# Optimization experiments

Measured on AMD Instinct MI355X. Metric: run time of the kernel, lower is better.

The kernel has to match this reference:

```python
import jax, jax.numpy as jnp
import numpy as np

H = 1024     # hidden_size
NH = 16      # num heads
HD = H // NH # head_dim = 64
I = 4096     # intermediate_size
EPS = 1e-6


def rmsnorm(x, w, eps=EPS):
    var = jnp.mean(jnp.square(x), axis=-1, keepdims=True)
    return x * jax.lax.rsqrt(var + eps) * w


def attention(x, ctx, wq, wk, wv, wo):
    # x: [B,S,H], ctx: [B,Skv,H]; weights stored [in,out]
    B, S, _ = x.shape
    Skv = ctx.shape[1]
    q = (x @ wq).reshape(B, S, NH, HD)
    k = (ctx @ wk).reshape(B, Skv, NH, HD)
    v = (ctx @ wv).reshape(B, Skv, NH, HD)
    scores = jnp.einsum('bqhd,bkhd->bhqk', q, k) * (HD ** -0.5)
    attn = jax.nn.softmax(scores.astype(jnp.float32), axis=-1).astype(q.dtype)
    out = jnp.einsum('bhqk,bkhd->bqhd', attn, v).reshape(B, S, NH * HD)
    return out @ wo


def mlp(x, wg, wu, wd):
    return (jax.nn.silu(x @ wg) * (x @ wu)) @ wd


def setup_inputs() -> dict:
    key = jax.random.key(0)
    ks = jax.random.split(key, 16)
    p = lambda k, shape: (jax.random.normal(k, shape, jnp.float32) * 0.02)
    return {
        'hidden_states': jax.random.normal(ks[0], (1, 2048, H), jnp.float32),
        'context': jax.random.normal(ks[1], (1, 2048, H), jnp.float32),
        'sa_norm_w': jnp.ones((H,), jnp.float32),
        'sa_wq': p(ks[2], (H, NH * HD)),
        'sa_wk': p(ks[3], (H, NH * HD)),
        'sa_wv': p(ks[4], (H, NH * HD)),
        'sa_wo': p(ks[5], (NH * HD, H)),
        'ca_norm_w': jnp.ones((H,), jnp.float32),
        'ca_wq': p(ks[6], (H, NH * HD)),
        'ca_wk': p(ks[7], (H, NH * HD)),
        'ca_wv': p(ks[8], (H, NH * HD)),
        'ca_wo': p(ks[9], (NH * HD, H)),
        'mlp_norm_w': jnp.ones((H,), jnp.float32),
        'w_gate': p(ks[10], (H, I)),
        'w_up': p(ks[11], (H, I)),
        'w_down': p(ks[12], (I, H)),
    }


def reference(hidden_states, context, sa_norm_w, sa_wq, sa_wk, sa_wv, sa_wo,
              ca_norm_w, ca_wq, ca_wk, ca_wv, ca_wo,
              mlp_norm_w, w_gate, w_up, w_down):
    # self-attention block
    residual = hidden_states
    h = rmsnorm(hidden_states, sa_norm_w)
    h = residual + attention(h, h, sa_wq, sa_wk, sa_wv, sa_wo)
    # cross-attention block
    residual = h
    hn = rmsnorm(h, ca_norm_w)
    h = residual + attention(hn, context, ca_wq, ca_wk, ca_wv, ca_wo)
    # MLP block
    residual = h
    hn = rmsnorm(h, mlp_norm_w)
    h = residual + mlp(hn, w_gate, w_up, w_down)
    return h
```

## Files before the change

### kernel.cpp

```cpp
#include <hip/hip_runtime.h>

#define H 1024
#define S 2048
#define NH 16
#define HD 64
#define ISZ 4096

typedef __attribute__((ext_vector_type(8))) short s8v;
typedef __attribute__((ext_vector_type(4))) short s4v;
typedef __attribute__((ext_vector_type(4))) float f4v;
typedef __attribute__((ext_vector_type(2))) unsigned u2v;

#define MFMA16 __builtin_amdgcn_mfma_f32_16x16x32_bf16

__device__ __forceinline__ short f2bf(float f) {
    unsigned u = __builtin_bit_cast(unsigned, f);
    unsigned r = (u + 0x7FFFu + ((u >> 16) & 1u)) >> 16;
    return (short)r;
}
__device__ __forceinline__ float bf2f(short s) {
    unsigned u = ((unsigned)(unsigned short)s) << 16;
    return __builtin_bit_cast(float, u);
}
__device__ __forceinline__ float exp2_hw(float x) {
    float r; asm("v_exp_f32 %0, %1" : "=v"(r) : "v"(x)); return r;
}
__device__ __forceinline__ unsigned cvt_pk_bf16(float lo, float hi) {
    unsigned r; asm("v_cvt_pk_bf16_f32 %0, %1, %2" : "=v"(r) : "v"(lo), "v"(hi)); return r;
}

__device__ __forceinline__ void gload_lds16(const short* g, short* l) {
    __builtin_amdgcn_global_load_lds(
        (const __attribute__((address_space(1))) void*)g,
        (__attribute__((address_space(3))) void*)l, 16, 0, 0);
}

template <int N> struct VMt { static constexpr int val = N; };

struct PreArgs {
    const void* hid; const void* ctx;
    const void* sanw; const void* canw; const void* mlpnw;
    const void* w[11];
    short* hidc; short* ctxc; short* xn;
    short* canw_o; short* mlpnw_o;
    short* wT[11];
    int* flag_out;
};

__device__ __forceinline__ void tr_tile(const void* src, short* dst, int K, int N,
                                        int k0, int n0, int rmul, int roff,
                                        int isbf, float* tile ) {
    int t = threadIdx.x;
    int c = t & 31, r0 = t >> 5;
    if (isbf) {
        const short* s = (const short*)src;
#pragma unroll
        for (int i = 0; i < 4; i++)
            tile[(r0 + i * 8) * 33 + c] = bf2f(s[(k0 + r0 + i * 8) * N + n0 + c]);
    } else {
        const float* s = (const float*)src;
#pragma unroll
        for (int i = 0; i < 4; i++)
            tile[(r0 + i * 8) * 33 + c] = s[(k0 + r0 + i * 8) * N + n0 + c];
    }
    __syncthreads();
#pragma unroll
    for (int i = 0; i < 4; i++)
        dst[((n0 + r0 + i * 8) * rmul + roff) * K + k0 + c] = f2bf(tile[c * 33 + r0 + i * 8]);
}

__global__ __launch_bounds__(256) void preamble_kernel(PreArgs pa) {
    __shared__ float tile[32 * 33];
    __shared__ float red[4];
    int b = blockIdx.x;
    int t = threadIdx.x;
    int isbf = (((const unsigned*)pa.sanw)[0] == 0x3F803F80u);
    if (blockIdx.x == 0 && t == 0) pa.flag_out[0] = isbf;

    if (b < 2048) {
        int row = b;
        float xf[4];
        if (isbf) {
            s4v xv = *(const s4v*)((const short*)pa.hid + row * H + t * 4);
#pragma unroll
            for (int j = 0; j < 4; j++) xf[j] = bf2f(xv[j]);
        } else {
            const float* s = (const float*)pa.hid + row * H + t * 4;
#pragma unroll
            for (int j = 0; j < 4; j++) xf[j] = s[j];
        }
        float ss = 0.f;
        s4v cv;
#pragma unroll
        for (int j = 0; j < 4; j++) { cv[j] = f2bf(xf[j]); xf[j] = bf2f(cv[j]); ss += xf[j] * xf[j]; }
        *(s4v*)(pa.hidc + row * H + t * 4) = cv;
        int lane = t & 63, wid = t >> 6;
#pragma unroll
        for (int off = 32; off >= 1; off >>= 1) ss += __shfl_xor(ss, off);
        if (lane == 0) red[wid] = ss;
        __syncthreads();
        float tot = red[0] + red[1] + red[2] + red[3];
        float scale = rsqrtf(tot * (1.f / (float)H) + 1e-6f);
        float wv[4];
        if (isbf) {
            s4v wq = *(const s4v*)((const short*)pa.sanw + t * 4);
#pragma unroll
            for (int j = 0; j < 4; j++) wv[j] = bf2f(wq[j]);
        } else {
            const float* s = (const float*)pa.sanw + t * 4;
#pragma unroll
            for (int j = 0; j < 4; j++) wv[j] = s[j];
        }
        s4v ov;
#pragma unroll
        for (int j = 0; j < 4; j++) ov[j] = f2bf(xf[j] * scale * wv[j]);
        *(s4v*)(pa.xn + row * H + t * 4) = ov;
        return;
    }
    b -= 2048;
    if (b < 1024) {
        int i8 = b * 2048 + t * 8;
        if (isbf) {
            *(s8v*)(pa.ctxc + i8) = *(const s8v*)((const short*)pa.ctx + i8);
        } else {
            const float* s = (const float*)pa.ctx;
            s8v o;
#pragma unroll
            for (int j = 0; j < 8; j++) o[j] = f2bf(s[i8 + j]);
            *(s8v*)(pa.ctxc + i8) = o;
        }
        return;
    }
    b -= 1024;
    if (b < 2) {
        const void* src = (b == 0) ? pa.canw : pa.mlpnw;
        short* dst = (b == 0) ? pa.canw_o : pa.mlpnw_o;
        if (isbf) { if (t * 4 < H) *(s4v*)(dst + t * 4) = *(const s4v*)((const short*)src + t * 4); }
        else {
            const float* s = (const float*)src;
            s4v o;
#pragma unroll
            for (int j = 0; j < 4; j++) o[j] = f2bf(s[t * 4 + j]);
            *(s4v*)(dst + t * 4) = o;
        }
        return;
    }
    b -= 2;
    if (b < 8 * 1024) {
        int w = b >> 10, tl = b & 1023;
        tr_tile(pa.w[w], pa.wT[w], H, H, (tl & 31) * 32, (tl >> 5) * 32, 1, 0, isbf, tile);
        return;
    }
    b -= 8 * 1024;
    if (b < 2 * 4096) {
        int w = 8 + (b >> 12), tl = b & 4095;
        tr_tile(pa.w[w], pa.wT[8], H, ISZ, (tl & 31) * 32, (tl >> 5) * 32, 2, w - 8, isbf, tile);
        return;
    }
    b -= 2 * 4096;
    {
        tr_tile(pa.w[10], pa.wT[10], ISZ, H, (b & 127) * 32, (b >> 7) * 32, 1, 0, isbf, tile);
    }
}

__global__ __launch_bounds__(256) void rmsnorm_kernel(const short* __restrict__ x,
                                                      const short* __restrict__ w,
                                                      short* __restrict__ out) {
    int row = blockIdx.x;
    int t = threadIdx.x;
    int lane = t & 63, wid = t >> 6;
    const short* xr = x + row * H;

    s4v xv = *(const s4v*)(xr + t * 4);
    float xf[4];
    float ss = 0.f;
#pragma unroll
    for (int j = 0; j < 4; j++) { xf[j] = bf2f(xv[j]); ss += xf[j] * xf[j]; }
#pragma unroll
    for (int off = 32; off >= 1; off >>= 1) ss += __shfl_xor(ss, off);

    __shared__ float red[4];
    if (lane == 0) red[wid] = ss;
    __syncthreads();
    float tot = red[0] + red[1] + red[2] + red[3];
    float scale = rsqrtf(tot * (1.f / (float)H) + 1e-6f);

    s4v wv = *(const s4v*)(w + t * 4);
    s4v ov;
#pragma unroll
    for (int j = 0; j < 4; j++) ov[j] = f2bf(xf[j] * scale * bf2f(wv[j]));
    *(s4v*)(out + row * H + t * 4) = ov;
}

template <int BM_, int BN_>
__global__ __launch_bounds__(512, 2) void gemm_bt_kernel(
    const short* __restrict__ A0, const short* __restrict__ A1, int split, int lda,
    const short* __restrict__ Bt,
    void* __restrict__ C, int ldc, int K,
    const short* __restrict__ res,
    const int* __restrict__ dtype_flag,
    short* __restrict__ vtbuf, int vcol0,
    short* __restrict__ silu_out) {

    constexpr int MC = BM_ / 32;
    constexpr int NC = BN_ / 64;
    constexpr int U  = (BM_ + BN_) / 8;
    constexpr int PT = U / 8;
    constexpr int BUF = (BM_ + BN_) * 64;

    __shared__ short lds[2 * BUF];

    const short* A = (blockIdx.y < split) ? A0 : A1;
    int m0 = blockIdx.x * BM_;
    int n0 = blockIdx.y * BN_;

    int t = threadIdx.x;
    int lane = t & 63, wid = t >> 6;
    int quad = lane >> 4, l15 = lane & 15;
    int wr = wid >> 2, wc = wid & 3;
    int ld4 = lane >> 2, lc8 = (lane & 3) * 8;

    f4v acc[MC][NC] = {};

    auto stage = [&](short* buf, int k0) {
#pragma unroll
        for (int s = 0; s < PT; ++s) {
            int u = wid * PT + s;
            if (u < BM_ / 8) {
                int h = u / (BM_ / 16), r16 = u % (BM_ / 16);
                gload_lds16(A + (m0 + r16 * 16 + ld4) * lda + k0 + h * 32 + lc8,
                            buf + h * (BM_ * 32) + r16 * 512);
            } else {
                int ub = u - BM_ / 8;
                int h = ub / (BN_ / 16), r16 = ub % (BN_ / 16);
                gload_lds16(Bt + (n0 + r16 * 16 + ld4) * K + k0 + h * 32 + lc8,
                            buf + BM_ * 64 + h * (BN_ * 32) + r16 * 512);
            }
        }
    };

    auto compute = [&](const short* buf) {
#pragma unroll
        for (int kh = 0; kh < 2; ++kh) {
            s8v af[MC], bfv[NC];
#pragma unroll
            for (int mc = 0; mc < MC; ++mc)
                af[mc] = *(const s8v*)(buf + kh * (BM_ * 32) +
                                       (wr * (BM_ / 2) + mc * 16 + l15) * 32 + quad * 8);
#pragma unroll
            for (int nc = 0; nc < NC; ++nc)
                bfv[nc] = *(const s8v*)(buf + BM_ * 64 + kh * (BN_ * 32) +
                                        (wc * (BN_ / 4) + nc * 16 + l15) * 32 + quad * 8);
#pragma unroll
            for (int mc = 0; mc < MC; ++mc)
#pragma unroll
                for (int nc = 0; nc < NC; ++nc)
                    acc[mc][nc] = MFMA16(af[mc], bfv[nc], acc[mc][nc], 0, 0, 0);
        }
    };

    const int KT = K / 64;
    stage(lds, 0);
    __syncthreads();
    int cur = 0;
    for (int kt = 0; kt < KT - 1; ++kt) {
        stage(lds + (cur ^ 1) * BUF, (kt + 1) * 64);
        compute(lds + cur * BUF);
        __syncthreads();
        cur ^= 1;
    }
    compute(lds + cur * BUF);

    if (silu_out) {
#pragma unroll
        for (int mc = 0; mc < MC; mc++) {
#pragma unroll
            for (int nc = 0; nc < NC; nc++) {
                int row = m0 + wr * (BM_ / 2) + mc * 16 + quad * 4;
                int col = n0 + wc * (BN_ / 4) + nc * 16 + l15;
#pragma unroll
                for (int r = 0; r < 4; r++) {
                    float v = acc[mc][nc][r];
                    float other = __shfl_xor(v, 1);
                    if ((l15 & 1) == 0) {
                        float sig = 1.f / (1.f + __expf(-v));
                        silu_out[(row + r) * ISZ + (col >> 1)] = f2bf(v * sig * other);
                    }
                }
            }
        }
        return;
    }

    int out_fp32 = (dtype_flag != nullptr) && (dtype_flag[0] == 0);

#pragma unroll
    for (int mc = 0; mc < MC; mc++) {
#pragma unroll
        for (int nc = 0; nc < NC; nc++) {
            int row = m0 + wr * (BM_ / 2) + mc * 16 + quad * 4;
            int col = n0 + wc * (BN_ / 4) + nc * 16 + l15;
#pragma unroll
            for (int r = 0; r < 4; r++) {
                float vf = acc[mc][nc][r];
                if (res) vf += bf2f(res[(row + r) * ldc + col]);
                if (vtbuf && col >= vcol0)
                    vtbuf[(col - vcol0) * S + row + r] = f2bf(vf);
                else if (out_fp32)
                    ((float*)C)[(row + r) * ldc + col] = vf;
                else
                    ((short*)C)[(row + r) * ldc + col] = f2bf(vf);
            }
        }
    }
}

template <int BM_, int BN_>
__global__ __launch_bounds__(512, 2) void gemm_np_kernel(
    const short* __restrict__ A, int lda,
    const short* __restrict__ Bt,
    void* __restrict__ C, int ldc, int K,
    const short* __restrict__ res,
    const int* __restrict__ dtype_flag) {

    constexpr int MC = BM_ / 32;
    constexpr int NC = BN_ / 64;
    constexpr int PT = (BM_ + BN_) / 64;
    constexpr int BUF = (BM_ + BN_) * 64;

    __shared__ short lds[4 * BUF];

    int lin = blockIdx.x;
    int sw = (lin & 7) * 32 + (lin >> 3);
    int m0 = (sw & 31) * BM_;
    int n0 = (sw >> 5) * BN_;

    int t_ = threadIdx.x;
    int lane = t_ & 63, wid = t_ >> 6;
    int quad = lane >> 4, l15 = lane & 15;
    int wr = wid >> 2, wc = wid & 3;
    int ld4 = lane >> 2;
    int lcs = (((lane & 3) ^ ((ld4 >> 1) & 3)) * 8);
    int sq  = quad ^ ((l15 >> 1) & 3);

    f4v acc[MC][NC] = {};

    auto stage = [&](int bi, int kt) {
        short* buf = lds + bi * BUF;
        int k0 = kt * 64;
#pragma unroll
        for (int s = 0; s < PT; ++s) {
            int u = wid * PT + s;
            if (u < BM_ / 8) {
                int hh = u / (BM_ / 16), r16 = u % (BM_ / 16);
                gload_lds16(A + (m0 + r16 * 16 + ld4) * lda + k0 + hh * 32 + lcs,
                            buf + hh * (BM_ * 32) + r16 * 512);
            } else {
                int ub = u - BM_ / 8;
                int hh = ub / (BN_ / 16), r16 = ub % (BN_ / 16);
                gload_lds16(Bt + (n0 + r16 * 16 + ld4) * K + k0 + hh * 32 + lcs,
                            buf + BM_ * 64 + hh * (BN_ * 32) + r16 * 512);
            }
        }
    };

    auto tile = [&](int t, auto wt) {
        constexpr int W = decltype(wt)::val;
        if constexpr (W == 9)      asm volatile("s_waitcnt vmcnt(9)" ::: "memory");
        else if constexpr (W == 6) asm volatile("s_waitcnt vmcnt(6)" ::: "memory");
        else if constexpr (W == 3) asm volatile("s_waitcnt vmcnt(3)" ::: "memory");
        else                       asm volatile("s_waitcnt vmcnt(0)" ::: "memory");
        __builtin_amdgcn_s_barrier();
        const short* bc = lds + (t & 3) * BUF;
        s8v af[2][MC], bv[2][NC];
#pragma unroll
        for (int kh = 0; kh < 2; ++kh) {
#pragma unroll
            for (int mc = 0; mc < MC; ++mc)
                af[kh][mc] = *(const s8v*)(bc + kh * (BM_ * 32) +
                                           (wr * (BM_ / 2) + mc * 16 + l15) * 32 + sq * 8);
#pragma unroll
            for (int nc = 0; nc < NC; ++nc)
                bv[kh][nc] = *(const s8v*)(bc + BM_ * 64 + kh * (BN_ * 32) +
                                           (wc * (BN_ / 4) + nc * 16 + l15) * 32 + sq * 8);
        }
        asm volatile("s_waitcnt lgkmcnt(0)" ::: "memory");
        __builtin_amdgcn_s_barrier();
        __builtin_amdgcn_s_setprio(1);
#pragma unroll
        for (int kh = 0; kh < 2; ++kh)
#pragma unroll
            for (int mc = 0; mc < MC; ++mc)
#pragma unroll
                for (int nc = 0; nc < NC; ++nc)
                    acc[mc][nc] = MFMA16(af[kh][mc], bv[kh][nc], acc[mc][nc], 0, 0, 0);
        __builtin_amdgcn_s_setprio(0);
    };

    const int KT = K / 64;
    stage(0, 0); stage(1, 1); stage(2, 2);
    for (int t = 0; t < KT - 3; ++t) {
        stage((t + 3) & 3, t + 3);
        tile(t, VMt<9>{});
    }
    tile(KT - 3, VMt<6>{});
    tile(KT - 2, VMt<3>{});
    tile(KT - 1, VMt<0>{});

    int out_fp32 = (dtype_flag != nullptr) && (dtype_flag[0] == 0);
#pragma unroll
    for (int mc = 0; mc < MC; mc++) {
#pragma unroll
        for (int nc = 0; nc < NC; nc++) {
            int row = m0 + wr * (BM_ / 2) + mc * 16 + quad * 4;
            int col = n0 + wc * (BN_ / 4) + nc * 16 + l15;
#pragma unroll
            for (int r = 0; r < 4; r++) {
                float vf = acc[mc][nc][r];
                if (res) vf += bf2f(res[(row + r) * ldc + col]);
                if (out_fp32)
                    ((float*)C)[(row + r) * ldc + col] = vf;
                else
                    ((short*)C)[(row + r) * ldc + col] = f2bf(vf);
            }
        }
    }
}

__global__ __launch_bounds__(512, 2) void gemm_gu8_kernel(
    const short* __restrict__ A, const short* __restrict__ Bt,
    short* __restrict__ silu_out) {

    __shared__ short lds[65536];

    int lin = blockIdx.x;
    int sw = (lin & 7) * 32 + (lin >> 3);
    int m0 = (sw & 7) * 256;
    int n0 = (sw >> 3) * 256;

    int t = threadIdx.x;
    int lane = t & 63, wid = t >> 6;
    int quad = lane >> 4, l15 = lane & 15;
    int wr = wid >> 2, wc = wid & 3;
    int ld4 = lane >> 2;
    int lcs = (((lane & 3) ^ ((ld4 >> 1) & 3)) * 8);
    int sq  = quad ^ ((l15 >> 1) & 3);

    f4v acc[8][4] = {};

    const short* Arow = A + (m0 + ld4) * 1024 + lcs;
    const short* Brow = Bt + (n0 + ld4) * 1024 + lcs;

    auto stA = [&](int buf, int kt, int kh) {
        short* d = lds + buf * 32768 + kh * 8192;
#pragma unroll
        for (int i = 0; i < 2; i++) {
            int r0 = (wid + 8 * i) * 16;
            gload_lds16(Arow + r0 * 1024 + kt * 64 + kh * 32, d + r0 * 32);
        }
    };
    auto stB = [&](int buf, int kt, int kh) {
        short* d = lds + buf * 32768 + 16384 + kh * 8192;
#pragma unroll
        for (int i = 0; i < 2; i++) {
            int r0 = (wid + 8 * i) * 16;
            gload_lds16(Brow + r0 * 1024 + kt * 64 + kh * 32, d + r0 * 32);
        }
    };

    const int aoff = (wr * 128 + l15) * 32 + sq * 8;
    const int boff = 16384 + (wc * 64 + l15) * 32 + sq * 8;

    stA(0, 0, 0); stB(0, 0, 0); stA(0, 0, 1); stB(0, 0, 1);
    asm volatile("s_waitcnt vmcnt(4)" ::: "memory");
    __builtin_amdgcn_s_barrier();

    int cur = 0;
    for (int kt = 0; kt < 15; ++kt) {
        const short* bc = lds + cur * 32768;
        int nb = cur ^ 1;
        s8v af[8], b0, b1;

#pragma unroll
        for (int mc = 0; mc < 8; ++mc) af[mc] = *(const s8v*)(bc + aoff + mc * 512);
        b0 = *(const s8v*)(bc + boff);
        b1 = *(const s8v*)(bc + boff + 512);
        stA(nb, kt + 1, 0);
        __builtin_amdgcn_s_barrier();
        asm volatile("s_waitcnt lgkmcnt(0)" ::: "memory");
        __builtin_amdgcn_s_setprio(1);
#pragma unroll
        for (int mc = 0; mc < 8; ++mc) {
            acc[mc][0] = MFMA16(af[mc], b0, acc[mc][0], 0, 0, 0);
            acc[mc][1] = MFMA16(af[mc], b1, acc[mc][1], 0, 0, 0);
        }
        __builtin_amdgcn_s_setprio(0);
        __builtin_amdgcn_s_barrier();

        b0 = *(const s8v*)(bc + boff + 1024);
        b1 = *(const s8v*)(bc + boff + 1536);
        stB(nb, kt + 1, 0);
        asm volatile("s_waitcnt vmcnt(4)" ::: "memory");
        __builtin_amdgcn_s_barrier();
        asm volatile("s_waitcnt lgkmcnt(0)" ::: "memory");
        __builtin_amdgcn_s_setprio(1);
#pragma unroll
        for (int mc = 0; mc < 8; ++mc) {
            acc[mc][2] = MFMA16(af[mc], b0, acc[mc][2], 0, 0, 0);
            acc[mc][3] = MFMA16(af[mc], b1, acc[mc][3], 0, 0, 0);
        }
        __builtin_amdgcn_s_setprio(0);
        __builtin_amdgcn_s_barrier();

#pragma unroll
        for (int mc = 0; mc < 8; ++mc) af[mc] = *(const s8v*)(bc + 8192 + aoff + mc * 512);
        b0 = *(const s8v*)(bc + 8192 + boff);
        b1 = *(const s8v*)(bc + 8192 + boff + 512);
        stA(nb, kt + 1, 1);
        __builtin_amdgcn_s_barrier();
        asm volatile("s_waitcnt lgkmcnt(0)" ::: "memory");
        __builtin_amdgcn_s_setprio(1);
#pragma unroll
        for (int mc = 0; mc < 8; ++mc) {
            acc[mc][0] = MFMA16(af[mc], b0, acc[mc][0], 0, 0, 0);
            acc[mc][1] = MFMA16(af[mc], b1, acc[mc][1], 0, 0, 0);
        }
        __builtin_amdgcn_s_setprio(0);
        __builtin_amdgcn_s_barrier();

        b0 = *(const s8v*)(bc + 8192 + boff + 1024);
        b1 = *(const s8v*)(bc + 8192 + boff + 1536);
        stB(nb, kt + 1, 1);
        asm volatile("s_waitcnt vmcnt(4)" ::: "memory");
        __builtin_amdgcn_s_barrier();
        asm volatile("s_waitcnt lgkmcnt(0)" ::: "memory");
        __builtin_amdgcn_s_setprio(1);
#pragma unroll
        for (int mc = 0; mc < 8; ++mc) {
            acc[mc][2] = MFMA16(af[mc], b0, acc[mc][2], 0, 0, 0);
            acc[mc][3] = MFMA16(af[mc], b1, acc[mc][3], 0, 0, 0);
        }
        __builtin_amdgcn_s_setprio(0);
        __builtin_amdgcn_s_barrier();

        cur ^= 1;
    }

    asm volatile("s_waitcnt vmcnt(0)" ::: "memory");
    __builtin_amdgcn_s_barrier();
    {
        const short* bc = lds + cur * 32768;
#pragma unroll
        for (int kh = 0; kh < 2; ++kh) {
            s8v af[8], bv[4];
#pragma unroll
            for (int mc = 0; mc < 8; ++mc) af[mc] = *(const s8v*)(bc + kh * 8192 + aoff + mc * 512);
#pragma unroll
            for (int nc = 0; nc < 4; ++nc) bv[nc] = *(const s8v*)(bc + kh * 8192 + boff + nc * 512);
#pragma unroll
            for (int mc = 0; mc < 8; ++mc)
#pragma unroll
                for (int nc = 0; nc < 4; ++nc)
                    acc[mc][nc] = MFMA16(af[mc], bv[nc], acc[mc][nc], 0, 0, 0);
        }
    }

#pragma unroll
    for (int mc = 0; mc < 8; mc++) {
#pragma unroll
        for (int nc = 0; nc < 4; nc++) {
            int row = m0 + wr * 128 + mc * 16 + quad * 4;
            int col = n0 + wc * 64 + nc * 16 + l15;
#pragma unroll
            for (int r = 0; r < 4; r++) {
                float v = acc[mc][nc][r];
                float other = __shfl_xor(v, 1);
                if ((l15 & 1) == 0) {
                    float sig = 1.f / (1.f + __expf(-v));
                    silu_out[(row + r) * ISZ + (col >> 1)] = f2bf(v * sig * other);
                }
            }
        }
    }
}

__global__ __launch_bounds__(512, 4) void flash_attn_kernel(const short* __restrict__ q,
                                                            const short* __restrict__ kk,
                                                            const short* __restrict__ vt,
                                                            int rs,
                                                            short* __restrict__ o) {
    __shared__ short lds[40960];

    int h = blockIdx.y;
    int q0 = blockIdx.x * 64;
    int t = threadIdx.x;
    int lane = t & 63, wid = t >> 6;
    int quad = lane >> 4, l15 = lane & 15;
    int gw = wid & 3, gh = wid >> 2;
    int kvbase = gh * 1024;
    int kro = l15 & 7;

    int lrow = lane >> 3;
    int lsrc = ((lane & 7) ^ lrow) * 8;

    auto stageKV = [&](int buf, int tt) {
        int kvt = kvbase + tt * 64;
        short* kb = lds + (gh * 2 + buf) * 4096;
        short* vb = lds + 16384 + (gh * 2 + buf) * 4096;
#pragma unroll
        for (int i = 0; i < 2; i++) {
            int r0 = gw * 16 + i * 8;
            gload_lds16(kk + (kvt + r0 + lrow) * rs + h * HD + lsrc, kb + r0 * 64);
            gload_lds16(vt + (h * HD + r0 + lrow) * S + kvt + lsrc, vb + r0 * 64);
        }
    };

    const float qscale = 0.125f * 1.44269504f;
    s8v bq[2];
    int qrow = q0 + gw * 16 + l15;
#pragma unroll
    for (int c = 0; c < 2; c++) {
        s8v raw = *(const s8v*)(q + qrow * rs + h * HD + c * 32 + quad * 8);
#pragma unroll
        for (int j = 0; j < 8; j++) bq[c][j] = f2bf(qscale * bf2f(raw[j]));
    }

    f4v o_acc[4] = {};
    float m_s = -INFINITY, l_s = 0.f;
    short* pw = lds + 32768 + wid * 1024;

    const int NT = 16;
    stageKV(0, 0);
    __syncthreads();
    int cur = 0;
    for (int tt = 0; tt < NT; ++tt) {
        if (tt + 1 < NT) stageKV(cur ^ 1, tt + 1);
        const short* kb = lds + (gh * 2 + cur) * 4096;
        const short* vb = lds + 16384 + (gh * 2 + cur) * 4096;

        f4v st[4];
#pragma unroll
        for (int kc = 0; kc < 4; kc++) {
            f4v a_ = (f4v){0.f, 0.f, 0.f, 0.f};
#pragma unroll
            for (int dc = 0; dc < 2; dc++) {
                s8v kf = *(const s8v*)(kb + (kc * 16 + l15) * 64 + ((dc * 4 + quad) ^ kro) * 8);
                a_ = MFMA16(kf, bq[dc], a_, 0, 0, 0);
            }
            st[kc] = a_;
        }

        float mloc = -INFINITY;
#pragma unroll
        for (int kc = 0; kc < 4; kc++)
#pragma unroll
            for (int r = 0; r < 4; r++) mloc = fmaxf(mloc, st[kc][r]);
        mloc = fmaxf(mloc, __shfl_xor(mloc, 16));
        mloc = fmaxf(mloc, __shfl_xor(mloc, 32));
        float m_new = fmaxf(m_s, mloc);
        float alpha = exp2_hw(m_s - m_new);
        float lloc = 0.f;
#pragma unroll
        for (int kc = 0; kc < 4; kc++)
#pragma unroll
            for (int r = 0; r < 4; r++) {
                float p = exp2_hw(st[kc][r] - m_new);
                st[kc][r] = p;
                lloc += p;
            }
        lloc += __shfl_xor(lloc, 16);
        lloc += __shfl_xor(lloc, 32);
        l_s = l_s * alpha + lloc;
        m_s = m_new;
#pragma unroll
        for (int nd = 0; nd < 4; nd++)
#pragma unroll
            for (int r = 0; r < 4; r++) o_acc[nd][r] *= alpha;

#pragma unroll
        for (int kc = 0; kc < 4; kc++) {
            u2v w;
            w[0] = cvt_pk_bf16(st[kc][0], st[kc][1]);
            w[1] = cvt_pk_bf16(st[kc][2], st[kc][3]);
            int pslot = (kc * 2 + (quad >> 1)) ^ kro;
            *(u2v*)(pw + l15 * 64 + pslot * 8 + (quad & 1) * 4) = w;
        }

#pragma unroll
        for (int nd = 0; nd < 4; nd++) {
#pragma unroll
            for (int kc2 = 0; kc2 < 2; kc2++) {
                s8v vf = *(const s8v*)(vb + (nd * 16 + l15) * 64 + ((kc2 * 4 + quad) ^ kro) * 8);
                s8v pf = *(const s8v*)(pw + l15 * 64 + ((kc2 * 4 + quad) ^ kro) * 8);
                o_acc[nd] = MFMA16(vf, pf, o_acc[nd], 0, 0, 0);
            }
        }
        __syncthreads();
        cur ^= 1;
    }

    float* ex = (float*)lds;
    if (gh == 1) {
        int base = (gw * 64 + lane) * 20;
#pragma unroll
        for (int nd = 0; nd < 4; nd++) *(f4v*)(ex + base + nd * 4) = o_acc[nd];
        ex[base + 16] = m_s;
        ex[base + 17] = l_s;
    }
    __syncthreads();
    if (gh == 1) return;

    int base = (wid * 64 + lane) * 20;
    float mB = ex[base + 16], lB = ex[base + 17];
    float M = fmaxf(m_s, mB);
    float a = exp2_hw(m_s - M), bsc = exp2_hw(mB - M);
    float inv = 1.f / (a * l_s + bsc * lB);
#pragma unroll
    for (int nd = 0; nd < 4; nd++) {
        f4v ob = *(const f4v*)(ex + base + nd * 4);
#pragma unroll
        for (int r = 0; r < 4; r++)
            o_acc[nd][r] = (a * o_acc[nd][r] + bsc * ob[r]) * inv;
    }

#pragma unroll
    for (int nd = 0; nd < 4; nd++)
#pragma unroll
        for (int r = 0; r < 4; r++)
            pw[l15 * 64 + nd * 16 + quad * 4 + r] = f2bf(o_acc[nd][r]);

    int qr = lane >> 2, dc2 = (lane & 3) * 16;
    s8v x0 = *(const s8v*)(pw + qr * 64 + dc2);
    s8v x1 = *(const s8v*)(pw + qr * 64 + dc2 + 8);
    short* dst = o + (q0 + wid * 16 + qr) * H + h * HD + dc2;
    *(s8v*)(dst) = x0;
    *(s8v*)(dst + 8) = x1;
}

extern "C" void kernel_launch(void* const* d_in, const int* in_sizes, int n_in,
                              void* d_out, int out_size, void* d_ws, size_t ws_size,
                              hipStream_t stream) {
    const int SH = S * H;
    const int WH = H * H;
    const int WI = H * ISZ;

    int* flag = (int*)d_ws;
    short* base = (short*)d_ws + 16;

    short* hidc   = base;
    short* ctxc   = hidc + SH;
    short* sanw   = ctxc + SH;
    short* canw   = sanw + H;
    short* mlpnw  = canw + H;
    short* saqkvT = mlpnw + H;
    short* sawoT  = saqkvT + 3 * WH;
    short* caqkvT = sawoT + WH;
    short* cawoT  = caqkvT + 3 * WH;
    short* wguT   = cawoT + WH;
    short* wdT    = wguT + 2 * WI;
    short* xn     = wdT + WI;
    short* qkv    = xn + SH;
    short* ao     = qkv + 3 * SH;
    short* h1     = ao + SH;
    short* gu     = qkv;
    short* h2     = qkv + 8 * SH;
    short* vt     = h2 + SH;

    dim3 blk(256);
    dim3 blk2(512);

    PreArgs pa;
    pa.hid = d_in[0]; pa.ctx = d_in[1];
    pa.sanw = d_in[2]; pa.canw = d_in[7]; pa.mlpnw = d_in[12];
    const void* wsrc[11] = {d_in[3], d_in[4], d_in[5], d_in[6],
                            d_in[8], d_in[9], d_in[10], d_in[11],
                            d_in[13], d_in[14], d_in[15]};
    short* wdst[11] = {saqkvT, saqkvT + WH, saqkvT + 2 * WH, sawoT,
                       caqkvT, caqkvT + WH, caqkvT + 2 * WH, cawoT,
                       wguT, wguT , wdT};
    for (int i = 0; i < 11; i++) { pa.w[i] = wsrc[i]; pa.wT[i] = wdst[i]; }
    pa.hidc = hidc; pa.ctxc = ctxc; pa.xn = xn;
    pa.canw_o = canw; pa.mlpnw_o = mlpnw;
    pa.flag_out = flag;
    const int pre_blocks = 2048 + 1024 + 2 + 8 * 1024 + 2 * 4096 + 4096;
    preamble_kernel<<<pre_blocks, blk, 0, stream>>>(pa);

    gemm_bt_kernel<128, 128><<<dim3(S / 128, 3 * H / 128), blk2, 0, stream>>>(
        xn, xn, 24, H, saqkvT, qkv, 3 * H, H, nullptr, nullptr, vt, 2 * H, nullptr);
    flash_attn_kernel<<<dim3(S / 64, NH), blk2, 0, stream>>>(qkv, qkv + H, vt, 3 * H, ao);
    gemm_np_kernel<64, 128><<<dim3(256), blk2, 0, stream>>>(
        ao, H, sawoT, h1, H, H, hidc, nullptr);

    rmsnorm_kernel<<<S, blk, 0, stream>>>(h1, canw, xn);
    gemm_bt_kernel<128, 128><<<dim3(S / 128, 3 * H / 128), blk2, 0, stream>>>(
        xn, ctxc, 8, H, caqkvT, qkv, 3 * H, H, nullptr, nullptr, vt, 2 * H, nullptr);
    flash_attn_kernel<<<dim3(S / 64, NH), blk2, 0, stream>>>(qkv, qkv + H, vt, 3 * H, ao);
    gemm_np_kernel<64, 128><<<dim3(256), blk2, 0, stream>>>(
        ao, H, cawoT, h2, H, H, h1, nullptr);

    rmsnorm_kernel<<<S, blk, 0, stream>>>(h2, mlpnw, xn);
    gemm_gu8_kernel<<<dim3(256), blk2, 0, stream>>>(xn, wguT, gu);
    gemm_np_kernel<64, 128><<<dim3(256), blk2, 0, stream>>>(
        gu, ISZ, wdT, d_out, H, ISZ, h2, flag);
}
```

Baseline: 424.5 us.

## Vectorize weight transpose tiles and pipeline QKV GEMM and attention with fine-grained waits

The weight-transpose preamble now moves 64x32 tiles with 16-byte vector loads and stores, which halves the block count and cuts per-element memory ops. The QKV GEMM is restructured to issue all LDS fragment loads before the MFMAs, uses explicit vmcnt/lgkmcnt waits with raw barriers instead of __syncthreads, raises wave priority during the MFMA section, and drops the unused silu epilogue. Flash attention swaps its full syncs for partial vmcnt waits so the next KV prefetch stays in flight. In gemm_gu8 the LDS XOR swizzle is removed, which may add LDS bank conflicts, and the hand-counted vmcnt values must match the number of outstanding loads.

Result: no change. 425.8 us (+0.3%).

```diff
diff --git a/kernel.cpp b/kernel.cpp
--- a/kernel.cpp
+++ b/kernel.cpp
@@ -51,26 +51,32 @@
                                         int k0, int n0, int rmul, int roff,
                                         int isbf, float* tile ) {
     int t = threadIdx.x;
-    int c = t & 31, r0 = t >> 5;
     if (isbf) {
         const short* s = (const short*)src;
-#pragma unroll
-        for (int i = 0; i < 4; i++)
-            tile[(r0 + i * 8) * 33 + c] = bf2f(s[(k0 + r0 + i * 8) * N + n0 + c]);
+        int r = t >> 2, c8 = (t & 3) * 8;
+        s8v v = *(const s8v*)(s + (k0 + r) * N + n0 + c8);
+#pragma unroll
+        for (int j = 0; j < 8; j++) tile[r * 33 + c8 + j] = bf2f(v[j]);
     } else {
         const float* s = (const float*)src;
-#pragma unroll
-        for (int i = 0; i < 4; i++)
-            tile[(r0 + i * 8) * 33 + c] = s[(k0 + r0 + i * 8) * N + n0 + c];
+        int r = t >> 2, c16 = (t & 3) * 8;
+#pragma unroll
+        for (int j = 0; j < 2; j++) {
+            f4v v = *(const f4v*)(s + (k0 + r) * N + n0 + c16 + j * 4);
+#pragma unroll
+            for (int e = 0; e < 4; e++) tile[r * 33 + c16 + j * 4 + e] = v[e];
+        }
     }
     __syncthreads();
-#pragma unroll
-    for (int i = 0; i < 4; i++)
-        dst[((n0 + r0 + i * 8) * rmul + roff) * K + k0 + c] = f2bf(tile[c * 33 + r0 + i * 8]);
+    int n = t >> 3, k8 = (t & 7) * 8;
+    short tmp[8];
+#pragma unroll
+    for (int e = 0; e < 8; e++) tmp[e] = f2bf(tile[(k8 + e) * 33 + n]);
+    *(s8v*)(dst + ((n0 + n) * rmul + roff) * K + k0 + k8) = *(s8v*)tmp;
 }
 
 __global__ __launch_bounds__(256) void preamble_kernel(PreArgs pa) {
-    __shared__ float tile[32 * 33];
+    __shared__ float tile[64 * 33];
     __shared__ float red[4];
     int b = blockIdx.x;
     int t = threadIdx.x;
@@ -146,20 +152,20 @@
         return;
     }
     b -= 2;
-    if (b < 8 * 1024) {
-        int w = b >> 10, tl = b & 1023;
-        tr_tile(pa.w[w], pa.wT[w], H, H, (tl & 31) * 32, (tl >> 5) * 32, 1, 0, isbf, tile);
+    if (b < 8 * 512) {
+        int w = b >> 9, tl = b & 511;
+        tr_tile(pa.w[w], pa.wT[w], H, H, (tl & 15) * 64, (tl >> 4) * 32, 1, 0, isbf, tile);
         return;
     }
-    b -= 8 * 1024;
-    if (b < 2 * 4096) {
-        int w = 8 + (b >> 12), tl = b & 4095;
-        tr_tile(pa.w[w], pa.wT[8], H, ISZ, (tl & 31) * 32, (tl >> 5) * 32, 2, w - 8, isbf, tile);
+    b -= 8 * 512;
+    if (b < 2 * 2048) {
+        int w = 8 + (b >> 11), tl = b & 2047;
+        tr_tile(pa.w[w], pa.wT[8], H, ISZ, (tl & 15) * 64, (tl >> 4) * 32, 2, w - 8, isbf, tile);
         return;
     }
-    b -= 2 * 4096;
+    b -= 2 * 2048;
     {
-        tr_tile(pa.w[10], pa.wT[10], ISZ, H, (b & 127) * 32, (b >> 7) * 32, 1, 0, isbf, tile);
+        tr_tile(pa.w[10], pa.wT[10], ISZ, H, (b & 63) * 64, (b >> 6) * 32, 1, 0, isbf, tile);
     }
 }
 
@@ -193,19 +199,17 @@
 }
 
 template <int BM_, int BN_>
-__global__ __launch_bounds__(512, 2) void gemm_bt_kernel(
+__global__ __launch_bounds__(512, 2) void gemm_qkv_kernel(
     const short* __restrict__ A0, const short* __restrict__ A1, int split, int lda,
     const short* __restrict__ Bt,
     void* __restrict__ C, int ldc, int K,
     const short* __restrict__ res,
     const int* __restrict__ dtype_flag,
-    short* __restrict__ vtbuf, int vcol0,
-    short* __restrict__ silu_out) {
+    short* __restrict__ vtbuf, int vcol0) {
 
     constexpr int MC = BM_ / 32;
     constexpr int NC = BN_ / 64;
-    constexpr int U  = (BM_ + BN_) / 8;
-    constexpr int PT = U / 8;
+    constexpr int PT = (BM_ + BN_) / 64;
     constexpr int BUF = (BM_ + BN_) * 64;
 
     __shared__ short lds[2 * BUF];
@@ -214,15 +218,17 @@
     int m0 = blockIdx.x * BM_;
     int n0 = blockIdx.y * BN_;
 
-    int t = threadIdx.x;
-    int lane = t & 63, wid = t >> 6;
+    int t_ = threadIdx.x;
+    int lane = t_ & 63, wid = t_ >> 6;
     int quad = lane >> 4, l15 = lane & 15;
     int wr = wid >> 2, wc = wid & 3;
     int ld4 = lane >> 2, lc8 = (lane & 3) * 8;
 
     f4v acc[MC][NC] = {};
 
-    auto stage = [&](short* buf, int k0) {
+    auto stage = [&](int bi, int kt) {
+        short* buf = lds + bi * BUF;
+        int k0 = kt * 64;
 #pragma unroll
         for (int s = 0; s < PT; ++s) {
             int u = wid * PT + s;
@@ -239,61 +245,46 @@
         }
     };
 
-    auto compute = [&](const short* buf) {
+    auto tile = [&](int t, auto wt) {
+        constexpr int W = decltype(wt)::val;
+        if constexpr (W == 4) asm volatile("s_waitcnt vmcnt(4)" ::: "memory");
+        else                  asm volatile("s_waitcnt vmcnt(0)" ::: "memory");
+        __builtin_amdgcn_s_barrier();
+        const short* bc = lds + (t & 1) * BUF;
+        s8v af[2][MC], bv[2][NC];
 #pragma unroll
         for (int kh = 0; kh < 2; ++kh) {
-            s8v af[MC], bfv[NC];
 #pragma unroll
             for (int mc = 0; mc < MC; ++mc)
-                af[mc] = *(const s8v*)(buf + kh * (BM_ * 32) +
-                                       (wr * (BM_ / 2) + mc * 16 + l15) * 32 + quad * 8);
+                af[kh][mc] = *(const s8v*)(bc + kh * (BM_ * 32) +
+                                           (wr * (BM_ / 2) + mc * 16 + l15) * 32 + quad * 8);
 #pragma unroll
             for (int nc = 0; nc < NC; ++nc)
-                bfv[nc] = *(const s8v*)(buf + BM_ * 64 + kh * (BN_ * 32) +
-                                        (wc * (BN_ / 4) + nc * 16 + l15) * 32 + quad * 8);
+                bv[kh][nc] = *(const s8v*)(bc + BM_ * 64 + kh * (BN_ * 32) +
+                                           (wc * (BN_ / 4) + nc * 16 + l15) * 32 + quad * 8);
+        }
+        asm volatile("s_waitcnt lgkmcnt(0)" ::: "memory");
+        __builtin_amdgcn_s_barrier();
+        __builtin_amdgcn_s_setprio(1);
+#pragma unroll
+        for (int kh = 0; kh < 2; ++kh)
 #pragma unroll
             for (int mc = 0; mc < MC; ++mc)
 #pragma unroll
                 for (int nc = 0; nc < NC; ++nc)
-                    acc[mc][nc] = MFMA16(af[mc], bfv[nc], acc[mc][nc], 0, 0, 0);
-        }
+                    acc[mc][nc] = MFMA16(af[kh][mc], bv[kh][nc], acc[mc][nc], 0, 0, 0);
+        __builtin_amdgcn_s_setprio(0);
     };
 
     const int KT = K / 64;
-    stage(lds, 0);
-    __syncthreads();
-    int cur = 0;
-    for (int kt = 0; kt < KT - 1; ++kt) {
-        stage(lds + (cur ^ 1) * BUF, (kt + 1) * 64);
-        compute(lds + cur * BUF);
-        __syncthreads();
-        cur ^= 1;
-    }
-    compute(lds + cur * BUF);
-
-    if (silu_out) {
-#pragma unroll
-        for (int mc = 0; mc < MC; mc++) {
-#pragma unroll
-            for (int nc = 0; nc < NC; nc++) {
-                int row = m0 + wr * (BM_ / 2) + mc * 16 + quad * 4;
-                int col = n0 + wc * (BN_ / 4) + nc * 16 + l15;
-#pragma unroll
-                for (int r = 0; r < 4; r++) {
-                    float v = acc[mc][nc][r];
-                    float other = __shfl_xor(v, 1);
-                    if ((l15 & 1) == 0) {
-                        float sig = 1.f / (1.f + __expf(-v));
-                        silu_out[(row + r) * ISZ + (col >> 1)] = f2bf(v * sig * other);
-                    }
-                }
-            }
-        }
-        return;
-    }
+    stage(0, 0);
+    for (int t = 0; t < KT - 1; ++t) {
+        stage((t + 1) & 1, t + 1);
+        tile(t, VMt<4>{});
+    }
+    tile(KT - 1, VMt<0>{});
 
     int out_fp32 = (dtype_flag != nullptr) && (dtype_flag[0] == 0);
-
 #pragma unroll
     for (int mc = 0; mc < MC; mc++) {
 #pragma unroll
@@ -442,14 +433,12 @@
     int lane = t & 63, wid = t >> 6;
     int quad = lane >> 4, l15 = lane & 15;
     int wr = wid >> 2, wc = wid & 3;
-    int ld4 = lane >> 2;
-    int lcs = (((lane & 3) ^ ((ld4 >> 1) & 3)) * 8);
-    int sq  = quad ^ ((l15 >> 1) & 3);
+    int ld4 = lane >> 2, lc8 = (lane & 3) * 8;
 
     f4v acc[8][4] = {};
 
-    const short* Arow = A + (m0 + ld4) * 1024 + lcs;
-    const short* Brow = Bt + (n0 + ld4) * 1024 + lcs;
+    const short* Arow = A + (m0 + ld4) * 1024 + lc8;
+    const short* Brow = Bt + (n0 + ld4) * 1024 + lc8;
 
     auto stA = [&](int buf, int kt, int kh) {
         short* d = lds + buf * 32768 + kh * 8192;
@@ -468,8 +457,8 @@
         }
     };
 
-    const int aoff = (wr * 128 + l15) * 32 + sq * 8;
-    const int boff = 16384 + (wc * 64 + l15) * 32 + sq * 8;
+    const int aoff = (wr * 128 + l15) * 32 + quad * 8;
+    const int boff = 16384 + (wc * 64 + l15) * 32 + quad * 8;
 
     stA(0, 0, 0); stB(0, 0, 0); stA(0, 0, 1); stB(0, 0, 1);
     asm volatile("s_waitcnt vmcnt(4)" ::: "memory");
@@ -631,10 +620,15 @@
 
     const int NT = 16;
     stageKV(0, 0);
-    __syncthreads();
     int cur = 0;
     for (int tt = 0; tt < NT; ++tt) {
-        if (tt + 1 < NT) stageKV(cur ^ 1, tt + 1);
+        if (tt + 1 < NT) {
+            stageKV(cur ^ 1, tt + 1);
+            asm volatile("s_waitcnt vmcnt(4)" ::: "memory");
+        } else {
+            asm volatile("s_waitcnt vmcnt(0)" ::: "memory");
+        }
+        __builtin_amdgcn_s_barrier();
         const short* kb = lds + (gh * 2 + cur) * 4096;
         const short* vb = lds + 16384 + (gh * 2 + cur) * 4096;
 
@@ -695,7 +689,8 @@
                 o_acc[nd] = MFMA16(vf, pf, o_acc[nd], 0, 0, 0);
             }
         }
-        __syncthreads();
+        asm volatile("s_waitcnt lgkmcnt(0)" ::: "memory");
+        __builtin_amdgcn_s_barrier();
         cur ^= 1;
     }
 
@@ -782,18 +777,18 @@
     pa.hidc = hidc; pa.ctxc = ctxc; pa.xn = xn;
     pa.canw_o = canw; pa.mlpnw_o = mlpnw;
     pa.flag_out = flag;
-    const int pre_blocks = 2048 + 1024 + 2 + 8 * 1024 + 2 * 4096 + 4096;
+    const int pre_blocks = 2048 + 1024 + 2 + 8 * 512 + 2 * 2048 + 2048;
     preamble_kernel<<<pre_blocks, blk, 0, stream>>>(pa);
 
-    gemm_bt_kernel<128, 128><<<dim3(S / 128, 3 * H / 128), blk2, 0, stream>>>(
-        xn, xn, 24, H, saqkvT, qkv, 3 * H, H, nullptr, nullptr, vt, 2 * H, nullptr);
+    gemm_qkv_kernel<128, 128><<<dim3(S / 128, 3 * H / 128), blk2, 0, stream>>>(
+        xn, xn, 24, H, saqkvT, qkv, 3 * H, H, nullptr, nullptr, vt, 2 * H);
     flash_attn_kernel<<<dim3(S / 64, NH), blk2, 0, stream>>>(qkv, qkv + H, vt, 3 * H, ao);
     gemm_np_kernel<64, 128><<<dim3(256), blk2, 0, stream>>>(
         ao, H, sawoT, h1, H, H, hidc, nullptr);
 
     rmsnorm_kernel<<<S, blk, 0, stream>>>(h1, canw, xn);
-    gemm_bt_kernel<128, 128><<<dim3(S / 128, 3 * H / 128), blk2, 0, stream>>>(
-        xn, ctxc, 8, H, caqkvT, qkv, 3 * H, H, nullptr, nullptr, vt, 2 * H, nullptr);
+    gemm_qkv_kernel<128, 128><<<dim3(S / 128, 3 * H / 128), blk2, 0, stream>>>(
+        xn, ctxc, 8, H, caqkvT, qkv, 3 * H, H, nullptr, nullptr, vt, 2 * H);
     flash_attn_kernel<<<dim3(S / 64, NH), blk2, 0, stream>>>(qkv, qkv + H, vt, 3 * H, ao);
     gemm_np_kernel<64, 128><<<dim3(256), blk2, 0, stream>>>(
         ao, H, cawoT, h2, H, H, h1, nullptr);
```
